# Kernel optimization log

Hardware: AMD Instinct MI355X
Metric: run time of the kernel (lower is better)

Reference implementation:

```python
import jax, jax.numpy as jnp
import numpy as np

B, L, D, H = 8, 512, 512, 8  # d_keys = d_values = d_model = D (default path)


def setup_inputs() -> dict:
    key = jax.random.key(0)
    ks = jax.random.split(key, 9)
    w = 0.02
    return {
        "queries": jax.random.normal(ks[0], (B, L, D), dtype=jnp.float32),
        "keys": jax.random.normal(ks[1], (B, L, D), dtype=jnp.float32),
        "values": jax.random.normal(ks[2], (B, L, D), dtype=jnp.float32),
        "Wq": jax.random.normal(ks[3], (D, D * H), dtype=jnp.float32) * w,
        "bq": jnp.zeros((D * H,), dtype=jnp.float32),
        "Wk": jax.random.normal(ks[4], (D, D * H), dtype=jnp.float32) * w,
        "bk": jnp.zeros((D * H,), dtype=jnp.float32),
        "Wv": jax.random.normal(ks[5], (D, D * H), dtype=jnp.float32) * w,
        "bv": jnp.zeros((D * H,), dtype=jnp.float32),
        "attn_mask": 0,  # must be falsy; original code would crash on a real tensor mask
    }


def reference(queries, keys, values, Wq, bq, Wk, bk, Wv, bv, attn_mask):
    b, l, d = queries.shape
    h = Wq.shape[1] // d
    # projections -> (B, L, H, E) with E = d_model
    q = (queries @ Wq + bq).reshape(b, l, h, d)
    k = (keys @ Wk + bk).reshape(b, l, h, d)
    v = (values @ Wv + bv).reshape(b, l, h, d)
    scale = 1.0 / np.sqrt(d).astype(np.float32)
    # per-position head-vs-head scores (B, L, H, H); equivalent to the i-loop
    s = jnp.einsum('blhe,blge->blhg', q, k) * scale
    p = jax.nn.softmax(s, axis=-1)
    # diagonal (l == i) contribution, summed over positions -> (B, H, E)
    attn_part = jnp.einsum('blhg,blge->bhe', p, v)
    # off-diagonal (l != i): uniform 1/H softmax of zero scores, (L-1) copies
    uniform_part = (jnp.float32(l - 1) / h) * v.sum(axis=(1, 2))  # (B, E)
    out = attn_part + uniform_part[:, None, :]  # (B, H, E)
    # final view(B, L, -1): requires L | H*E
    return out.reshape(b, l, -1)
```

## Files before the change

### kernel.cpp

```cpp
#include <hip/hip_runtime.h>


using f32x4 = __attribute__((ext_vector_type(4))) float;

__device__ __forceinline__ float bflo(unsigned int u) {
    union { unsigned int u; float f; } c; c.u = u << 16; return c.f;
}

#define GLOAD16(gp, lp) __builtin_amdgcn_global_load_lds( \
    (const __attribute__((address_space(1))) unsigned int*)(gp), \
    (__attribute__((address_space(3))) unsigned int*)(lp), 16, 0, 0)

__global__ __launch_bounds__(256) void prep(
    const float* __restrict__ x0, const float* __restrict__ x1,
    unsigned char* __restrict__ o0, unsigned char* __restrict__ o1,
    const float* __restrict__ w0, const float* __restrict__ w1,
    unsigned char* __restrict__ t0, unsigned char* __restrict__ t1)
{
    const int z = blockIdx.z;
    if (z < 2) {
        const float* src = (z == 0) ? x0 : x1;
        unsigned char* dst = (z == 0) ? o0 : o1;
        int i = (blockIdx.x * 256 + threadIdx.x) * 8;
        if (i < 2097152) {
            float4 a = *(const float4*)(src + i);
            float4 b = *(const float4*)(src + i + 4);
            uint2 u;
            u.x = __builtin_amdgcn_cvt_pk_fp8_f32(a.x, a.y, 0u, false);
            u.x = __builtin_amdgcn_cvt_pk_fp8_f32(a.z, a.w, u.x, true);
            u.y = __builtin_amdgcn_cvt_pk_fp8_f32(b.x, b.y, 0u, false);
            u.y = __builtin_amdgcn_cvt_pk_fp8_f32(b.z, b.w, u.y, true);
            *(uint2*)(dst + i) = u;
        }
    } else {
        const float* W = (z == 2) ? w0 : w1;
        unsigned char* T = (z == 2) ? t0 : t1;
        __shared__ float tile[32][33];
        const int n0 = (blockIdx.x & 127) * 32, k0 = (blockIdx.x >> 7) * 32;
        const int tx = threadIdx.x & 31, ty = threadIdx.x >> 5;
        #pragma unroll
        for (int j = 0; j < 32; j += 8)
            tile[ty + j][tx] = W[(size_t)(k0 + ty + j) * 4096 + n0 + tx];
        __syncthreads();
        const int n = ty * 4 + (tx >> 3), kq = tx & 7;
        unsigned int pk = __builtin_amdgcn_cvt_pk_fp8_f32(
            16.f * tile[kq * 4 + 0][n], 16.f * tile[kq * 4 + 1][n], 0u, false);
        pk = __builtin_amdgcn_cvt_pk_fp8_f32(
            16.f * tile[kq * 4 + 2][n], 16.f * tile[kq * 4 + 3][n], pk, true);
        *(unsigned int*)(T + (size_t)(n0 + n) * 512 + k0 + kq * 4) = pk;
    }
}

__global__ __launch_bounds__(512) void gemm_bt256(
    const unsigned char* __restrict__ a0, const unsigned char* __restrict__ a1,
    const unsigned char* __restrict__ w0, const unsigned char* __restrict__ w1,
    const float* __restrict__ b0, const float* __restrict__ b1,
    unsigned char* __restrict__ c0, unsigned char* __restrict__ c1)
{
    const unsigned char* A;  const unsigned char* Bt; const float* bias; unsigned char* C;
    if (blockIdx.z == 0) { A = a0; Bt = w0; bias = b0; C = c0; }
    else                 { A = a1; Bt = w1; bias = b1; C = c1; }

    __shared__ __align__(16) unsigned char SH[65536];

    const int tid  = threadIdx.x;
    const int lane = tid & 63;
    const int wid  = tid >> 6;
    const int wr   = wid >> 2;
    const int wn   = wid & 3;
    const int linb = blockIdx.y * 16 + blockIdx.x;
    const int swz  = (linb & 7) * 32 + (linb >> 3);
    const int bx   = (swz >> 6) * 4 + (swz & 3);
    const int by   = (swz >> 2) & 15;
    const int row0 = by * 256;
    const int n0   = bx * 256;

    const int lgs = (tid & 7) ^ ((tid >> 3) & 7);
    const int shi = lgs >> 2, slo = lgs & 3;
    const int srow0 = (tid >> 3) + shi * 128;
    const unsigned char* gA = A  + (size_t)(row0 + srow0) * 512 + slo * 16;
    const unsigned char* gB = Bt + (size_t)(n0   + srow0) * 512 + slo * 16;

#define STAGE_A(gp, buf, c, trel)                                                 \
    GLOAD16((gp) + (c) * (64 * 512) + (trel) * 64,                                \
            SH + (buf) * 16384 + (c) * 8192 + wid * 1024)
#define STAGE_B(gp, buf, c, trel)                                                 \
    GLOAD16((gp) + (c) * (64 * 512) + (trel) * 64,                                \
            SH + 32768 + (buf) * 16384 + (c) * 8192 + wid * 1024)

    const int l7 = lane & 7, koh = lane >> 5, kol = (lane >> 4) & 1, l15 = lane & 15;
    const char* bA0 = (const char*)SH + l15 * 128 + (((0 * 2 + koh + wr * 4) ^ l7) << 4) + kol * 8;
    const char* bA1 = (const char*)SH + l15 * 128 + (((1 * 2 + koh + wr * 4) ^ l7) << 4) + kol * 8;
    const char* bB0 = (const char*)SH + 32768 + (wn & 1) * 8192 + l15 * 128
                      + (((0 * 2 + koh + (wn >> 1) * 4) ^ l7) << 4) + kol * 8;
    const char* bB1 = (const char*)SH + 32768 + (wn & 1) * 8192 + l15 * 128
                      + (((1 * 2 + koh + (wn >> 1) * 4) ^ l7) << 4) + kol * 8;

#define LD_A(c, m, s) (*(const long long*)(((s) ? bA1 : bA0) + (c) * 16384 + (m) * 2048))
#define LD_B(c, n, s) (*(const long long*)(((s) ? bB1 : bB0) + (c) * 16384 + (n) * 2048))

#define BAR() __builtin_amdgcn_s_barrier()
#define VMC2() asm volatile("s_waitcnt vmcnt(2)" ::: "memory")
#define VMC0() asm volatile("s_waitcnt vmcnt(0)" ::: "memory")

    f32x4 acc[8][4];
    #pragma unroll
    for (int m = 0; m < 8; ++m)
        #pragma unroll
        for (int n = 0; n < 4; ++n)
            acc[m][n] = (f32x4){0.f, 0.f, 0.f, 0.f};

    long long bfr[4][2];
    long long fa0, fa1, fa2, fa3;

#define LDA_Q(c, q) { fa0 = LD_A(c, 2*(q), 0);   fa1 = LD_A(c, 2*(q), 1);         \
                      fa2 = LD_A(c, 2*(q)+1, 0); fa3 = LD_A(c, 2*(q)+1, 1); }
#define LDB_ALL(c) { _Pragma("unroll") for (int n = 0; n < 4; ++n) {              \
                       bfr[n][0] = LD_B(c, n, 0); bfr[n][1] = LD_B(c, n, 1); } }
#define MFMA_Q(q) { __builtin_amdgcn_s_setprio(1);                                \
    _Pragma("unroll") for (int n = 0; n < 4; ++n) {                               \
      acc[2*(q)][n]   = __builtin_amdgcn_mfma_f32_16x16x32_fp8_fp8(bfr[n][0], fa0, acc[2*(q)][n],   0,0,0); \
      acc[2*(q)][n]   = __builtin_amdgcn_mfma_f32_16x16x32_fp8_fp8(bfr[n][1], fa1, acc[2*(q)][n],   0,0,0); \
      acc[2*(q)+1][n] = __builtin_amdgcn_mfma_f32_16x16x32_fp8_fp8(bfr[n][0], fa2, acc[2*(q)+1][n], 0,0,0); \
      acc[2*(q)+1][n] = __builtin_amdgcn_mfma_f32_16x16x32_fp8_fp8(bfr[n][1], fa3, acc[2*(q)+1][n], 0,0,0); } \
    __builtin_amdgcn_s_setprio(0); }

    STAGE_B(gB, 0, 0, 0); STAGE_B(gB, 0, 1, 0);
    STAGE_A(gA, 0, 0, 0); STAGE_A(gA, 0, 1, 0);
    STAGE_B(gB, 1, 0, 1); STAGE_B(gB, 1, 1, 1);
    VMC2();
    BAR();

    const unsigned char* gAt = gA;
    const unsigned char* gBt = gB;
    for (int i = 0; i < 4; ++i) {
        const bool s23 = (i < 3);

        LDA_Q(0, 0); LDB_ALL(0);
        STAGE_A(gAt, 1, 0, 1);
        BAR(); MFMA_Q(0); BAR();

        LDA_Q(0, 1);
        STAGE_A(gAt, 1, 1, 1);
        BAR(); MFMA_Q(1); BAR();

        LDA_Q(0, 2);
        if (s23) STAGE_B(gBt, 0, 0, 2);
        BAR(); MFMA_Q(2); BAR();

        LDA_Q(0, 3);
        if (s23) STAGE_B(gBt, 0, 1, 2);
        BAR(); MFMA_Q(3);
        if (s23) { VMC2(); } else { VMC0(); }
        BAR();

        LDA_Q(1, 0); LDB_ALL(1);
        if (s23) STAGE_A(gAt, 0, 0, 2);
        BAR(); MFMA_Q(0); BAR();

        LDA_Q(1, 1);
        if (s23) STAGE_A(gAt, 0, 1, 2);
        BAR(); MFMA_Q(1); BAR();

        LDA_Q(1, 2);
        if (s23) STAGE_B(gBt, 1, 0, 3);
        BAR(); MFMA_Q(2); BAR();

        LDA_Q(1, 3);
        if (s23) STAGE_B(gBt, 1, 1, 3);
        BAR(); MFMA_Q(3);
        if (s23) { VMC2(); }
        BAR();

        gAt += 128; gBt += 128;
    }

    {
        const int q  = lane >> 4;
        const int tr = wr * 128 + (lane & 15);
        #pragma unroll
        for (int n = 0; n < 4; ++n) {
            float4 bb = *(const float4*)(bias + n0 + wn * 64 + n * 16 + q * 4);
            const int g16 = wn * 4 + n;
            #pragma unroll
            for (int m = 0; m < 8; ++m) {
                const int trm = tr + m * 16;
                unsigned int pk = __builtin_amdgcn_cvt_pk_fp8_f32(
                    acc[m][n][0] + 16.f * bb.x, acc[m][n][1] + 16.f * bb.y, 0u, false);
                pk = __builtin_amdgcn_cvt_pk_fp8_f32(
                    acc[m][n][2] + 16.f * bb.z, acc[m][n][3] + 16.f * bb.w, pk, true);
                *(unsigned int*)(SH + trm * 256 + ((g16 ^ (trm & 15)) << 4) + q * 4) = pk;
            }
        }
        BAR();
        #pragma unroll
        for (int it = 0; it < 8; ++it) {
            const int f = it * 512 + tid;
            const int rr = f >> 4, gg = f & 15;
            uint4 v = *(const uint4*)(SH + rr * 256 + ((gg ^ (rr & 15)) << 4));
            *(uint4*)(C + (size_t)(row0 + rr) * 4096 + gg * 16 + n0) = v;
        }
    }
#undef STAGE_A
#undef STAGE_B
#undef LD_A
#undef LD_B
}

__global__ __launch_bounds__(256) void mfscores(const unsigned char* __restrict__ Q,
                                                const unsigned char* __restrict__ K,
                                                float* __restrict__ P,
                                                float* __restrict__ pbpart)
{
    __shared__ float Pl[8 * 64];
    const int b = blockIdx.x, lc = blockIdx.y;
    const int tid = threadIdx.x, lane = tid & 63, w = tid >> 6;
    const int l0 = lc * 8;

    const int colr = lane & 15;
    const int ko   = lane >> 4;
    const int la   = l0 + w * 2 + (colr >> 3);
    const int hh   = colr & 7;
    const unsigned char* qrow = Q + (size_t)(b * 512 + la) * 4096 + hh * 512 + ko * 8;
    const unsigned char* krow = K + (size_t)(b * 512 + la) * 4096 + hh * 512 + ko * 8;

    f32x4 acc = (f32x4){0.f, 0.f, 0.f, 0.f};
    #pragma unroll
    for (int kt = 0; kt < 16; ++kt) {
        long long av = *(const long long*)(qrow + kt * 32);
        long long bv = *(const long long*)(krow + kt * 32);
        acc = __builtin_amdgcn_mfma_f32_16x16x32_fp8_fp8(av, bv, acc, 0, 0, 0);
    }

    const int lpr = ko >> 1;
    const int lpc = (lane >> 3) & 1;
    #pragma unroll
    for (int r = 0; r < 4; ++r) {
        float s = acc[r] * 1.7263349150062e-4f;
        float m = s;
        m = fmaxf(m, __shfl_xor(m, 1));
        m = fmaxf(m, __shfl_xor(m, 2));
        m = fmaxf(m, __shfl_xor(m, 4));
        float e = __expf(s - m);
        float ss = e;
        ss += __shfl_xor(ss, 1);
        ss += __shfl_xor(ss, 2);
        ss += __shfl_xor(ss, 4);
        float p = e / ss + 63.875f;
        if (lpr == lpc)
            Pl[(w * 2 + lpr) * 64 + ((ko & 1) * 4 + r) * 8 + (lane & 7)] = p;
    }
    __syncthreads();

    {
        const int l = tid >> 5, off = (tid & 31) * 2;
        float2 v = *(const float2*)&Pl[l * 64 + off];
        *(float2*)(P + (size_t)(b * 512 + l0 + l) * 64 + off) = v;
    }
    if (tid < 64) {
        float s = 0.f;
        #pragma unroll
        for (int l = 0; l < 8; ++l) s += Pl[l * 64 + tid];
        pbpart[((size_t)b * 64 + lc) * 64 + tid] = s;
    }
}

__global__ __launch_bounds__(256) void ykern(const float* __restrict__ P,
                                             const float* __restrict__ Xv,
                                             float* __restrict__ ypart)
{
    __shared__ float Pl[128 * 64];
    __shared__ float Xl[128 * 64];
    const int b = blockIdx.x, dt = blockIdx.y, lc = blockIdx.z;
    const int tid = threadIdx.x;
    const int tm = tid & 15, te = tid >> 4;

    const float* Pg = P + ((size_t)b * 512 + lc * 128) * 64;
    #pragma unroll
    for (int i = 0; i < 8; ++i)
        *(float4*)&Pl[(i * 256 + tid) * 4] = *(const float4*)(Pg + (size_t)(i * 256 + tid) * 4);
    const float* Xg = Xv + ((size_t)b * 512 + lc * 128) * 512 + dt * 64;
    #pragma unroll
    for (int i = 0; i < 8; ++i) {
        int flat = i * 256 + tid;
        int r = flat >> 4, q = flat & 15;
        *(float4*)&Xl[r * 64 + q * 4] = *(const float4*)(Xg + (size_t)r * 512 + q * 4);
    }
    __syncthreads();

    float4 acc[4];
    #pragma unroll
    for (int i = 0; i < 4; ++i) acc[i] = make_float4(0.f, 0.f, 0.f, 0.f);

    for (int l = 0; l < 128; ++l) {
        float4 pv = *(const float4*)&Pl[l * 64 + tm * 4];
        float4 xv = *(const float4*)&Xl[l * 64 + te * 4];
        acc[0].x += pv.x * xv.x; acc[0].y += pv.x * xv.y; acc[0].z += pv.x * xv.z; acc[0].w += pv.x * xv.w;
        acc[1].x += pv.y * xv.x; acc[1].y += pv.y * xv.y; acc[1].z += pv.y * xv.z; acc[1].w += pv.y * xv.w;
        acc[2].x += pv.z * xv.x; acc[2].y += pv.z * xv.y; acc[2].z += pv.z * xv.z; acc[2].w += pv.z * xv.w;
        acc[3].x += pv.w * xv.x; acc[3].y += pv.w * xv.y; acc[3].z += pv.w * xv.z; acc[3].w += pv.w * xv.w;
    }
    #pragma unroll
    for (int i = 0; i < 4; ++i)
        *(float4*)&ypart[(((size_t)lc * 8 + b) * 64 + tm * 4 + i) * 512 + dt * 64 + te * 4] = acc[i];
}

__global__ __launch_bounds__(256) void vgemm(const float* __restrict__ ypart,
                                             const float* __restrict__ Wv,
                                             float* __restrict__ partial)
{
    __shared__ float Al[64 * 64];
    __shared__ float Bl[64 * 64];
    const int et = blockIdx.x, kc = blockIdx.y;
    const int g = kc >> 3, d0 = (kc & 7) * 64, e0 = et * 64;
    const int tid = threadIdx.x;
    const int tm = tid & 15, te = tid >> 4;

    #pragma unroll
    for (int i = 0; i < 4; ++i) {
        int flat = i * 256 + tid;
        int bh = flat >> 4, dq = flat & 15;
        int yrow = (bh >> 3) * 64 + (bh & 7) * 8 + g;
        size_t base = ((size_t)(yrow >> 6) * 64 + (yrow & 63)) * 512 + d0 + dq * 4;
        float4 v = *(const float4*)(ypart + base);
        #pragma unroll
        for (int lc = 1; lc < 4; ++lc) {
            float4 t = *(const float4*)(ypart + (size_t)lc * 262144 + base);
            v.x += t.x; v.y += t.y; v.z += t.z; v.w += t.w;
        }
        *(float4*)&Al[bh * 64 + ((dq ^ (bh >> 2)) << 2)] = v;
    }
    #pragma unroll
    for (int i = 0; i < 4; ++i) {
        int flat = i * 256 + tid;
        int kk = flat >> 4, eq = flat & 15;
        *(float4*)&Bl[kk * 64 + eq * 4] =
            *(const float4*)(Wv + (size_t)(d0 + kk) * 4096 + g * 512 + e0 + eq * 4);
    }
    __syncthreads();

    float4 acc[4];
    #pragma unroll
    for (int j = 0; j < 4; ++j) acc[j] = make_float4(0.f, 0.f, 0.f, 0.f);

    for (int k = 0; k < 64; ++k) {
        float4 b4 = *(const float4*)&Bl[k * 64 + te * 4];
        const int gcol = (((k >> 2) ^ tm) << 2) + (k & 3);
        #pragma unroll
        for (int j = 0; j < 4; ++j) {
            float a = Al[(tm * 4 + j) * 64 + gcol];
            acc[j].x += a * b4.x; acc[j].y += a * b4.y;
            acc[j].z += a * b4.z; acc[j].w += a * b4.w;
        }
    }
    #pragma unroll
    for (int j = 0; j < 4; ++j)
        *(float4*)&partial[(size_t)kc * 32768 + (tm * 4 + j) * 512 + e0 + te * 4] = acc[j];
}

__global__ __launch_bounds__(256) void finalize(const float* __restrict__ partial,
                                                const float* __restrict__ pbpart,
                                                const float* __restrict__ bv,
                                                float* __restrict__ out)
{
    __shared__ float csh[8];
    const int blk = blockIdx.x;
    const int tid = threadIdx.x;
    const int b = blk >> 4, h = (blk >> 1) & 7;
    const int e = (blk & 1) * 256 + tid;

    if (tid < 8) {
        float s = 0.f;
        #pragma unroll 8
        for (int lcc = 0; lcc < 64; ++lcc)
            s += pbpart[((size_t)b * 64 + lcc) * 64 + h * 8 + tid];
        csh[tid] = s;
    }
    __syncthreads();

    const int i = ((b * 8 + h) << 9) + e;
    float s = 0.f;
    #pragma unroll
    for (int kc = 0; kc < 64; ++kc) s += partial[(size_t)kc * 32768 + i];
    float bt = 0.f;
    #pragma unroll
    for (int g = 0; g < 8; ++g) bt += csh[g] * bv[g * 512 + e];
    out[i] = s + bt;
}

extern "C" void kernel_launch(void* const* d_in, const int* in_sizes, int n_in,
                              void* d_out, int out_size, void* d_ws, size_t ws_size,
                              hipStream_t stream)
{
    const float* queries = (const float*)d_in[0];
    const float* keys    = (const float*)d_in[1];
    const float* values  = (const float*)d_in[2];
    const float* Wq      = (const float*)d_in[3];
    const float* bq      = (const float*)d_in[4];
    const float* Wk      = (const float*)d_in[5];
    const float* bk      = (const float*)d_in[6];
    const float* Wv      = (const float*)d_in[7];
    const float* bv      = (const float*)d_in[8];

    unsigned char* xq  = (unsigned char*)d_ws;
    unsigned char* xk  = xq  + (1u << 21);
    unsigned char* wtq = xk  + (1u << 21);
    unsigned char* wtk = wtq + (1u << 21);
    unsigned char* Q   = wtk + (1u << 21);
    unsigned char* Kb  = Q   + (1u << 24);
    float* P      = (float*)(Kb + (1u << 24));
    float* pbpart = P + 262144;
    float* ypart  = pbpart + 32768;
    float* part   = ypart + 4 * 262144;

    prep<<<dim3(2048, 1, 4), 256, 0, stream>>>(queries, keys, xq, xk, Wq, Wk, wtq, wtk);
    gemm_bt256<<<dim3(16, 16, 2), 512, 0, stream>>>(xq, xk, wtq, wtk, bq, bk, Q, Kb);
    mfscores<<<dim3(8, 64), 256, 0, stream>>>(Q, Kb, P, pbpart);
    ykern<<<dim3(8, 8, 4), 256, 0, stream>>>(P, values, ypart);
    vgemm<<<dim3(8, 64), 256, 0, stream>>>(ypart, Wv, part);
    finalize<<<dim3(128), 256, 0, stream>>>(part, pbpart, bv, (float*)d_out);
}
```

Measured before the change: 81.02 us.

## Fuse score softmax and P·V reduction into one kernel

```diff
diff --git a/kernel.cpp b/kernel.cpp
--- a/kernel.cpp
+++ b/kernel.cpp
@@ -2,10 +2,6 @@
 
 
 using f32x4 = __attribute__((ext_vector_type(4))) float;
-
-__device__ __forceinline__ float bflo(unsigned int u) {
-    union { unsigned int u; float f; } c; c.u = u << 16; return c.f;
-}
 
 #define GLOAD16(gp, lp) __builtin_amdgcn_global_load_lds( \
     (const __attribute__((address_space(1))) unsigned int*)(gp), \
@@ -207,102 +203,89 @@
 #undef LD_B
 }
 
-__global__ __launch_bounds__(256) void mfscores(const unsigned char* __restrict__ Q,
-                                                const unsigned char* __restrict__ K,
-                                                float* __restrict__ P,
-                                                float* __restrict__ pbpart)
-{
-    __shared__ float Pl[8 * 64];
-    const int b = blockIdx.x, lc = blockIdx.y;
+__global__ __launch_bounds__(512) void scores_y(
+    const unsigned char* __restrict__ Q, const unsigned char* __restrict__ K,
+    const float* __restrict__ Xv, float* __restrict__ ypart, float* __restrict__ cpart)
+{
+    __shared__ float Pl[64 * 64];
+    __shared__ float Xl[64 * 64];
+    __shared__ float red[512];
+    const int b = blockIdx.x, dt = blockIdx.y, zh = blockIdx.z;
     const int tid = threadIdx.x, lane = tid & 63, w = tid >> 6;
-    const int l0 = lc * 8;
-
-    const int colr = lane & 15;
-    const int ko   = lane >> 4;
-    const int la   = l0 + w * 2 + (colr >> 3);
-    const int hh   = colr & 7;
-    const unsigned char* qrow = Q + (size_t)(b * 512 + la) * 4096 + hh * 512 + ko * 8;
-    const unsigned char* krow = K + (size_t)(b * 512 + la) * 4096 + hh * 512 + ko * 8;
-
-    f32x4 acc = (f32x4){0.f, 0.f, 0.f, 0.f};
-    #pragma unroll
-    for (int kt = 0; kt < 16; ++kt) {
-        long long av = *(const long long*)(qrow + kt * 32);
-        long long bv = *(const long long*)(krow + kt * 32);
-        acc = __builtin_amdgcn_mfma_f32_16x16x32_fp8_fp8(av, bv, acc, 0, 0, 0);
-    }
-
-    const int lpr = ko >> 1;
-    const int lpc = (lane >> 3) & 1;
-    #pragma unroll
-    for (int r = 0; r < 4; ++r) {
-        float s = acc[r] * 1.7263349150062e-4f;
-        float m = s;
-        m = fmaxf(m, __shfl_xor(m, 1));
-        m = fmaxf(m, __shfl_xor(m, 2));
-        m = fmaxf(m, __shfl_xor(m, 4));
-        float e = __expf(s - m);
-        float ss = e;
-        ss += __shfl_xor(ss, 1);
-        ss += __shfl_xor(ss, 2);
-        ss += __shfl_xor(ss, 4);
-        float p = e / ss + 63.875f;
-        if (lpr == lpc)
-            Pl[(w * 2 + lpr) * 64 + ((ko & 1) * 4 + r) * 8 + (lane & 7)] = p;
-    }
+    const int colr = lane & 15, ko = lane >> 4;
+    const int lpr = ko >> 1, lpc = (lane >> 3) & 1;
+    const int tm = tid & 15, td = tid >> 4;
+    const int rq = tid >> 6, col = tid & 63;
+
+    float yacc[4][2];
+    #pragma unroll
+    for (int i = 0; i < 4; ++i) { yacc[i][0] = 0.f; yacc[i][1] = 0.f; }
+    float pbacc = 0.f;
+
+    for (int cc = 0; cc < 2; ++cc) {
+        const int l0 = zh * 128 + cc * 64;
+        #pragma unroll
+        for (int pp = 0; pp < 4; ++pp) {
+            const int p = w * 4 + pp;
+            const size_t la = (size_t)(b * 512 + l0 + 2 * p + (colr >> 3));
+            const unsigned char* qrow = Q + la * 4096 + (colr & 7) * 512 + ko * 8;
+            const unsigned char* krow = K + la * 4096 + (colr & 7) * 512 + ko * 8;
+            f32x4 acc = (f32x4){0.f, 0.f, 0.f, 0.f};
+            #pragma unroll
+            for (int kt = 0; kt < 16; ++kt) {
+                long long av = *(const long long*)(qrow + kt * 32);
+                long long bv = *(const long long*)(krow + kt * 32);
+                acc = __builtin_amdgcn_mfma_f32_16x16x32_fp8_fp8(av, bv, acc, 0, 0, 0);
+            }
+            #pragma unroll
+            for (int r = 0; r < 4; ++r) {
+                float s = acc[r] * 1.7263349150062e-4f;
+                float m = s;
+                m = fmaxf(m, __shfl_xor(m, 1));
+                m = fmaxf(m, __shfl_xor(m, 2));
+                m = fmaxf(m, __shfl_xor(m, 4));
+                float e = __expf(s - m);
+                float ss = e;
+                ss += __shfl_xor(ss, 1);
+                ss += __shfl_xor(ss, 2);
+                ss += __shfl_xor(ss, 4);
+                float pv = e / ss + 63.875f;
+                if (lpr == lpc)
+                    Pl[(2 * p + lpr) * 64 + ((ko & 1) * 4 + r) * 8 + (lane & 7)] = pv;
+            }
+        }
+        #pragma unroll
+        for (int it = 0; it < 2; ++it) {
+            int f = it * 512 + tid;
+            int r = f >> 4, q = f & 15;
+            *(float4*)&Xl[r * 64 + q * 4] =
+                *(const float4*)(Xv + (size_t)(b * 512 + l0 + r) * 512 + dt * 64 + q * 4);
+        }
+        __syncthreads();
+        #pragma unroll
+        for (int j = 0; j < 8; ++j) pbacc += Pl[(rq * 8 + j) * 64 + col];
+        for (int l = 0; l < 64; ++l) {
+            float4 pv = *(const float4*)&Pl[l * 64 + tm * 4];
+            float2 xv = *(const float2*)&Xl[l * 64 + td * 2];
+            yacc[0][0] += pv.x * xv.x; yacc[0][1] += pv.x * xv.y;
+            yacc[1][0] += pv.y * xv.x; yacc[1][1] += pv.y * xv.y;
+            yacc[2][0] += pv.z * xv.x; yacc[2][1] += pv.z * xv.y;
+            yacc[3][0] += pv.w * xv.x; yacc[3][1] += pv.w * xv.y;
+        }
+        __syncthreads();
+    }
+    #pragma unroll
+    for (int i = 0; i < 4; ++i)
+        *(float2*)&ypart[(((size_t)zh * 8 + b) * 64 + tm * 4 + i) * 512 + dt * 64 + td * 2]
+            = make_float2(yacc[i][0], yacc[i][1]);
+    red[tid] = pbacc;
     __syncthreads();
-
-    {
-        const int l = tid >> 5, off = (tid & 31) * 2;
-        float2 v = *(const float2*)&Pl[l * 64 + off];
-        *(float2*)(P + (size_t)(b * 512 + l0 + l) * 64 + off) = v;
-    }
-    if (tid < 64) {
+    if (dt == 0 && tid < 64) {
         float s = 0.f;
         #pragma unroll
-        for (int l = 0; l < 8; ++l) s += Pl[l * 64 + tid];
-        pbpart[((size_t)b * 64 + lc) * 64 + tid] = s;
-    }
-}
-
-__global__ __launch_bounds__(256) void ykern(const float* __restrict__ P,
-                                             const float* __restrict__ Xv,
-                                             float* __restrict__ ypart)
-{
-    __shared__ float Pl[128 * 64];
-    __shared__ float Xl[128 * 64];
-    const int b = blockIdx.x, dt = blockIdx.y, lc = blockIdx.z;
-    const int tid = threadIdx.x;
-    const int tm = tid & 15, te = tid >> 4;
-
-    const float* Pg = P + ((size_t)b * 512 + lc * 128) * 64;
-    #pragma unroll
-    for (int i = 0; i < 8; ++i)
-        *(float4*)&Pl[(i * 256 + tid) * 4] = *(const float4*)(Pg + (size_t)(i * 256 + tid) * 4);
-    const float* Xg = Xv + ((size_t)b * 512 + lc * 128) * 512 + dt * 64;
-    #pragma unroll
-    for (int i = 0; i < 8; ++i) {
-        int flat = i * 256 + tid;
-        int r = flat >> 4, q = flat & 15;
-        *(float4*)&Xl[r * 64 + q * 4] = *(const float4*)(Xg + (size_t)r * 512 + q * 4);
-    }
-    __syncthreads();
-
-    float4 acc[4];
-    #pragma unroll
-    for (int i = 0; i < 4; ++i) acc[i] = make_float4(0.f, 0.f, 0.f, 0.f);
-
-    for (int l = 0; l < 128; ++l) {
-        float4 pv = *(const float4*)&Pl[l * 64 + tm * 4];
-        float4 xv = *(const float4*)&Xl[l * 64 + te * 4];
-        acc[0].x += pv.x * xv.x; acc[0].y += pv.x * xv.y; acc[0].z += pv.x * xv.z; acc[0].w += pv.x * xv.w;
-        acc[1].x += pv.y * xv.x; acc[1].y += pv.y * xv.y; acc[1].z += pv.y * xv.z; acc[1].w += pv.y * xv.w;
-        acc[2].x += pv.z * xv.x; acc[2].y += pv.z * xv.y; acc[2].z += pv.z * xv.z; acc[2].w += pv.z * xv.w;
-        acc[3].x += pv.w * xv.x; acc[3].y += pv.w * xv.y; acc[3].z += pv.w * xv.z; acc[3].w += pv.w * xv.w;
-    }
-    #pragma unroll
-    for (int i = 0; i < 4; ++i)
-        *(float4*)&ypart[(((size_t)lc * 8 + b) * 64 + tm * 4 + i) * 512 + dt * 64 + te * 4] = acc[i];
+        for (int q = 0; q < 8; ++q) s += red[q * 64 + tid];
+        cpart[((size_t)zh * 8 + b) * 64 + tid] = s;
+    }
 }
 
 __global__ __launch_bounds__(256) void vgemm(const float* __restrict__ ypart,
@@ -359,7 +342,7 @@
 }
 
 __global__ __launch_bounds__(256) void finalize(const float* __restrict__ partial,
-                                                const float* __restrict__ pbpart,
+                                                const float* __restrict__ cpart,
                                                 const float* __restrict__ bv,
                                                 float* __restrict__ out)
 {
@@ -371,9 +354,9 @@
 
     if (tid < 8) {
         float s = 0.f;
-        #pragma unroll 8
-        for (int lcc = 0; lcc < 64; ++lcc)
-            s += pbpart[((size_t)b * 64 + lcc) * 64 + h * 8 + tid];
+        #pragma unroll
+        for (int zh = 0; zh < 4; ++zh)
+            s += cpart[((size_t)zh * 8 + b) * 64 + h * 8 + tid];
         csh[tid] = s;
     }
     __syncthreads();
@@ -408,15 +391,13 @@
     unsigned char* wtk = wtq + (1u << 21);
     unsigned char* Q   = wtk + (1u << 21);
     unsigned char* Kb  = Q   + (1u << 24);
-    float* P      = (float*)(Kb + (1u << 24));
-    float* pbpart = P + 262144;
-    float* ypart  = pbpart + 32768;
-    float* part   = ypart + 4 * 262144;
+    float* ypart = (float*)(Kb + (1u << 24));
+    float* cpart = ypart + 4 * 262144;
+    float* part  = cpart + 2048;
 
     prep<<<dim3(2048, 1, 4), 256, 0, stream>>>(queries, keys, xq, xk, Wq, Wk, wtq, wtk);
     gemm_bt256<<<dim3(16, 16, 2), 512, 0, stream>>>(xq, xk, wtq, wtk, bq, bk, Q, Kb);
-    mfscores<<<dim3(8, 64), 256, 0, stream>>>(Q, Kb, P, pbpart);
-    ykern<<<dim3(8, 8, 4), 256, 0, stream>>>(P, values, ypart);
+    scores_y<<<dim3(8, 8, 4), 512, 0, stream>>>(Q, Kb, values, ypart, cpart);
     vgemm<<<dim3(8, 64), 256, 0, stream>>>(ypart, Wv, part);
-    finalize<<<dim3(128), 256, 0, stream>>>(part, pbpart, bv, (float*)d_out);
-}
+    finalize<<<dim3(128), 256, 0, stream>>>(part, cpart, bv, (float*)d_out);
+}
```

Result: slower. 127.3 us (+57.2%).
